# Kernel tuning notes

Measured on AMD Instinct MI355X. Metric: run time of the kernel, lower is better.

Reference implementation:

```python
import jax, jax.numpy as jnp
import numpy as np

B, T, C, H = 4, 4096, 2048, 128  # batch, seq, emb_dim, head_size


def setup_inputs() -> dict:
    key = jax.random.key(0)
    k1, k2, k3, k4 = jax.random.split(key, 4)
    idx = jax.random.normal(k1, (B, T, C), dtype=jnp.float32)
    # nn.Linear weight layout: [out_features, in_features]; scale like torch init
    s = 1.0 / np.sqrt(C)
    Wq = jax.random.uniform(k2, (H, C), jnp.float32, -s, s)
    Wk = jax.random.uniform(k3, (H, C), jnp.float32, -s, s)
    Wv = jax.random.uniform(k4, (H, C), jnp.float32, -s, s)
    return {"idx": idx, "Wq": Wq, "Wk": Wk, "Wv": Wv}


def reference(idx, Wq, Wk, Wv):
    b, t, c = idx.shape
    q = jnp.einsum('btc,hc->bth', idx, Wq)  # [B,T,H]
    k = jnp.einsum('btc,hc->bth', idx, Wk)
    v = jnp.einsum('btc,hc->bth', idx, Wv)
    # NOTE: original computes keys @ queries^T and scales by emb_dim**-0.5
    scale = jnp.asarray(c, idx.dtype) ** -0.5
    wei = jnp.einsum('bih,bjh->bij', k, q) * scale  # [B,T,T]
    causal = jnp.tril(jnp.ones((t, t), dtype=bool))
    wei = jnp.where(causal, wei, -jnp.inf)
    wei = jax.nn.softmax(wei, axis=-1)
    return jnp.einsum('bij,bjh->bih', wei, v)  # [B,T,H]
```

## Files before the change

kernel.cpp:

```cpp
#include <hip/hip_runtime.h>
#include <hip/hip_bf16.h>
#include <cstdint>

#define TSEQ 4096
#define CDIM 2048
#define HDIM 128

typedef short bf8v __attribute__((ext_vector_type(8)));
typedef float f4v  __attribute__((ext_vector_type(4)));

__device__ __forceinline__ unsigned short f2b(float f) {
  union { float f; unsigned u; } v; v.f = f;
  unsigned u = v.u;
  return (unsigned short)((u + 0x7fffu + ((u >> 16) & 1u)) >> 16);
}

__device__ __forceinline__ f4v mfma16(bf8v a, bf8v b, f4v c) {
  return __builtin_amdgcn_mfma_f32_16x16x32_bf16(a, b, c, 0, 0, 0);
}

__device__ __forceinline__ void gload_lds16(const void* g, void* l) {
  __builtin_amdgcn_global_load_lds(
      (const __attribute__((address_space(1))) unsigned int*)g,
      (__attribute__((address_space(3))) unsigned int*)l, 16, 0, 0);
}

__global__ void wcat_kernel(const float* __restrict__ Wq, const float* __restrict__ Wk,
                            const float* __restrict__ Wv, unsigned short* __restrict__ Wcat) {
  int e = (blockIdx.x * 256 + threadIdx.x) * 4;
  int n = e >> 11;
  int k = e & 2047;
  const float* src;
  if (n < 128)      src = Wq + (size_t)n * CDIM + k;
  else if (n < 256) src = Wk + (size_t)(n - 128) * CDIM + k;
  else              src = Wv + (size_t)(n - 256) * CDIM + k;
  float4 f = *(const float4*)src;
  ushort4 o;
  o.x = f2b(f.x); o.y = f2b(f.y); o.z = f2b(f.z); o.w = f2b(f.w);
  *(ushort4*)(Wcat + e) = o;
}

__global__ __launch_bounds__(512, 6) void proj_gemm(const float* __restrict__ A,
                                                    const unsigned short* __restrict__ Bw,
                                                    unsigned short* __restrict__ QB,
                                                    unsigned short* __restrict__ KA,
                                                    unsigned short* __restrict__ VB) {
  __shared__ union {
    struct { unsigned short As[2][64][72]; unsigned short Bs[2][128][64]; } st;
    unsigned short Ct[64][132];
  } sm;
  const int m0 = blockIdx.x * 64;
  const int y  = blockIdx.y;
  const int n0g = y * 128;
  const int tid = threadIdx.x;
  const int lane = tid & 63;
  const int w = tid >> 6;
  const int wm = (w & 1) * 32, wn = (w >> 1) * 32;
  const int llo = lane & 15, lhi = lane >> 4;

  f4v acc[2][2];
#pragma unroll
  for (int i = 0; i < 2; ++i)
#pragma unroll
    for (int j = 0; j < 2; ++j) acc[i][j] = (f4v){0.f, 0.f, 0.f, 0.f};

  const int ar0 = tid >> 4;
  const int ac0 = (tid & 15) * 4;
  const float* aptr0 = A + (size_t)(m0 + ar0) * CDIM + ac0;
  const float* aptr1 = A + (size_t)(m0 + 32 + ar0) * CDIM + ac0;

  const int brow = lane >> 3;
  const int bgs  = (lane & 7) ^ brow;
  const unsigned short* bptr = Bw + (size_t)(n0g + w * 16 + brow) * CDIM + bgs * 8;

  float4 fa0 = *(const float4*)(aptr0);
  float4 fa1 = *(const float4*)(aptr1);
  gload_lds16(bptr,            &sm.st.Bs[0][w * 16][0]);
  gload_lds16(bptr + 8 * CDIM, &sm.st.Bs[0][w * 16 + 8][0]);
  {
    ushort4 o0, o1;
    o0.x = f2b(fa0.x); o0.y = f2b(fa0.y); o0.z = f2b(fa0.z); o0.w = f2b(fa0.w);
    o1.x = f2b(fa1.x); o1.y = f2b(fa1.y); o1.z = f2b(fa1.z); o1.w = f2b(fa1.w);
    *(ushort4*)&sm.st.As[0][ar0][ac0]      = o0;
    *(ushort4*)&sm.st.As[0][32 + ar0][ac0] = o1;
  }

  for (int it = 0; it < 32; ++it) {
    const int cur = it & 1;
    __syncthreads();
    if (it < 31) {
      fa0 = *(const float4*)(aptr0 + (it + 1) * 64);
      fa1 = *(const float4*)(aptr1 + (it + 1) * 64);
      const int nxt = cur ^ 1;
      gload_lds16(bptr + (it + 1) * 64,            &sm.st.Bs[nxt][w * 16][0]);
      gload_lds16(bptr + 8 * CDIM + (it + 1) * 64, &sm.st.Bs[nxt][w * 16 + 8][0]);
    }
#pragma unroll
    for (int kk = 0; kk < 2; ++kk) {
      bf8v af[2], bfr[2];
      af[0] = *(const bf8v*)&sm.st.As[cur][wm + llo][kk * 32 + lhi * 8];
      af[1] = *(const bf8v*)&sm.st.As[cur][wm + 16 + llo][kk * 32 + lhi * 8];
      const int bofs = (((kk << 2) + lhi) ^ (llo & 7)) * 8;
      bfr[0] = *(const bf8v*)&sm.st.Bs[cur][wn + llo][bofs];
      bfr[1] = *(const bf8v*)&sm.st.Bs[cur][wn + 16 + llo][bofs];
#pragma unroll
      for (int i = 0; i < 2; ++i)
#pragma unroll
        for (int j = 0; j < 2; ++j) acc[i][j] = mfma16(af[i], bfr[j], acc[i][j]);
    }
    if (it < 31) {
      const int nxt = cur ^ 1;
      ushort4 o0, o1;
      o0.x = f2b(fa0.x); o0.y = f2b(fa0.y); o0.z = f2b(fa0.z); o0.w = f2b(fa0.w);
      o1.x = f2b(fa1.x); o1.y = f2b(fa1.y); o1.z = f2b(fa1.z); o1.w = f2b(fa1.w);
      *(ushort4*)&sm.st.As[nxt][ar0][ac0]      = o0;
      *(ushort4*)&sm.st.As[nxt][32 + ar0][ac0] = o1;
    }
  }
  __syncthreads();
#pragma unroll
  for (int i = 0; i < 2; ++i)
#pragma unroll
    for (int j = 0; j < 2; ++j)
#pragma unroll
      for (int r = 0; r < 4; ++r)
        sm.Ct[wm + i * 16 + lhi * 4 + r][wn + j * 16 + llo] = f2b(acc[i][j][r]);
  __syncthreads();
  if (y < 2) {
    unsigned short* dst = (y == 0) ? QB : KA;
    const size_t base16 = (size_t)(m0 >> 4);
#pragma unroll
    for (int p = 0; p < 2; ++p) {
      int g = p * 512 + tid;
      int t16l = g >> 8, kk = (g >> 6) & 3, ln = g & 63;
      int lo = ln & 15, hi = ln >> 4;
      bf8v v = *(const bf8v*)&sm.Ct[t16l * 16 + lo][kk * 32 + hi * 8];
      *(bf8v*)(dst + (((base16 + t16l) * 4 + kk) * 64 + ln) * 8) = v;
    }
  } else {
    const size_t base32 = (size_t)(m0 >> 5);
#pragma unroll
    for (int p = 0; p < 3; ++p) {
      int g = p * 512 + tid;
      if (g < 1152) {
        int jbl = g / 576;
        int ht  = (g % 576) >> 6;
        int ln  = g & 63;
        int lo = ln & 15, hi = ln >> 4;
        bf8v v;
        if (ht == 8) {
#pragma unroll
          for (int e = 0; e < 8; ++e) v[e] = (lo == 0) ? (short)0x3F80 : (short)0;
        } else {
#pragma unroll
          for (int e = 0; e < 8; ++e) v[e] = (short)sm.Ct[jbl * 32 + hi * 8 + e][ht * 16 + lo];
        }
        *(bf8v*)(VB + (((base32 + jbl) * 9 + ht) * 512 + (size_t)ln * 8)) = v;
      }
    }
  }
}

__global__ __launch_bounds__(256, 4) void attn6(const unsigned short* __restrict__ QB,
                                                const unsigned short* __restrict__ KA,
                                                const unsigned short* __restrict__ VB,
                                                float* __restrict__ out) {
  __shared__ union SM {
    unsigned short Ps[4][2][16][68];
    struct { float Om[4][16][68]; float Lm[4][16]; } mg;
  } sm;
  const int x = blockIdx.x;
  const int b = x & 3;
  const int u = x >> 2;
  const int g = u >> 6, r0 = u & 63;
  const int s = (g & 1) ? (g * 64 + 63 - r0) : (g * 64 + r0);
  const int lastjt = s >> 2;
  const int tid = threadIdx.x;
  const int w = tid >> 6, lane = tid & 63;
  const int llo = lane & 15, lhi = lane >> 4;
  const float scale = 0.022097086912079608f;

  bf8v aK[4];
  {
    const unsigned short* kp = KA + (size_t)(b * 256 + s) * 2048;
#pragma unroll
    for (int kk = 0; kk < 4; ++kk) aK[kk] = *(const bf8v*)(kp + (kk * 64 + lane) * 8);
  }

  f4v Oacc[9];
#pragma unroll
  for (int nt = 0; nt < 9; ++nt) Oacc[nt] = (f4v){0.f, 0.f, 0.f, 0.f};

  auto computeS = [&](int jtS, int buf) {
    const unsigned short* qp = QB + (size_t)(b * 256 + jtS * 4) * 2048;
#pragma unroll
    for (int ct = 0; ct < 4; ++ct) {
      f4v acc = (f4v){0.f, 0.f, 0.f, 0.f};
#pragma unroll
      for (int kk = 0; kk < 4; ++kk) {
        bf8v bq = *(const bf8v*)(qp + ((ct * 4 + kk) * 64 + lane) * 8);
        acc = mfma16(aK[kk], bq, acc);
      }
#pragma unroll
      for (int r = 0; r < 4; ++r) {
        float sv = acc[r];
        if (jtS == lastjt) {
          int j = jtS * 64 + ct * 16 + llo;
          int i = s * 16 + lhi * 4 + r;
          if (j > i) sv = -3.0e38f;
        }
        sm.Ps[w][buf][lhi * 4 + r][ct * 16 + llo] = f2b(__expf(sv * scale));
      }
    }
  };

  if (w <= lastjt) computeS(w, 0);
  int buf = 0;
  for (int jt = w; jt <= lastjt; jt += 4) {
    bf8v aP0 = *(const bf8v*)&sm.Ps[w][buf][llo][lhi * 8];
    bf8v aP1 = *(const bf8v*)&sm.Ps[w][buf][llo][32 + lhi * 8];
    if (jt + 4 <= lastjt) computeS(jt + 4, buf ^ 1);
    const unsigned short* vp = VB + (size_t)(b * 128 + jt * 2) * 4608;
#pragma unroll
    for (int nt = 0; nt < 9; ++nt) {
      f4v o = Oacc[nt];
      o = mfma16(aP0, *(const bf8v*)(vp + nt * 512 + (size_t)lane * 8), o);
      o = mfma16(aP1, *(const bf8v*)(vp + 4608 + nt * 512 + (size_t)lane * 8), o);
      Oacc[nt] = o;
    }
    buf ^= 1;
  }

#pragma unroll
  for (int half = 0; half < 2; ++half) {
    __syncthreads();
#pragma unroll
    for (int nt = 0; nt < 4; ++nt)
#pragma unroll
      for (int r = 0; r < 4; ++r)
        sm.mg.Om[w][lhi * 4 + r][nt * 16 + llo] = Oacc[half * 4 + nt][r];
    if (half == 0 && llo == 0) {
#pragma unroll
      for (int r = 0; r < 4; ++r) sm.mg.Lm[w][lhi * 4 + r] = Oacc[8][r];
    }
    __syncthreads();
    {
      int row = tid >> 4, c0 = (tid & 15) * 4;
      float L = sm.mg.Lm[0][row] + sm.mg.Lm[1][row] + sm.mg.Lm[2][row] + sm.mg.Lm[3][row];
      float inv = 1.0f / L;
      float* op = out + (size_t)(b * TSEQ + s * 16 + row) * HDIM + half * 64 + c0;
#pragma unroll
      for (int e = 0; e < 4; ++e) {
        float o = sm.mg.Om[0][row][c0 + e] + sm.mg.Om[1][row][c0 + e] +
                  sm.mg.Om[2][row][c0 + e] + sm.mg.Om[3][row][c0 + e];
        op[e] = o * inv;
      }
    }
  }
}

extern "C" void kernel_launch(void* const* d_in, const int* in_sizes, int n_in,
                              void* d_out, int out_size, void* d_ws, size_t ws_size,
                              hipStream_t stream) {
  const float* idx = (const float*)d_in[0];
  const float* Wq  = (const float*)d_in[1];
  const float* Wk  = (const float*)d_in[2];
  const float* Wv  = (const float*)d_in[3];
  float* out = (float*)d_out;
  char* ws = (char*)d_ws;
  unsigned short* Wcat = (unsigned short*)ws;
  unsigned short* QB   = (unsigned short*)(ws + ((size_t)2  << 20));
  unsigned short* KA   = (unsigned short*)(ws + ((size_t)7  << 20));
  unsigned short* VB   = (unsigned short*)(ws + ((size_t)12 << 20));

  wcat_kernel<<<768, 256, 0, stream>>>(Wq, Wk, Wv, Wcat);
  proj_gemm<<<dim3(256, 3), 512, 0, stream>>>(idx, Wcat, QB, KA, VB);
  attn6<<<1024, 256, 0, stream>>>(QB, KA, VB, out);
}
```

Before: 286.2 us.

## Process two query row tiles per attention block to reuse Q and V loads

The attention kernel now gives each block two adjacent 16-row tiles, and loads each Q and V fragment once to feed both tiles' MFMAs. This halves global and L2 traffic for Q and V per unit of work. The grid is halved, with a new pairing scheme to balance causal work, and launch bounds drop to two blocks per SM to fit the doubled registers. Separately, the projection GEMM's float-to-bf16 conversion uses the packed v_cvt_pk_bf16_f32 instruction instead of manual rounding. The cost is higher register pressure and lower occupancy, and the last tile of each pair does some masked extra work.

Result: slower. 300.9 us (+5.1%).

```diff
diff --git a/kernel.cpp b/kernel.cpp
--- a/kernel.cpp
+++ b/kernel.cpp
@@ -13,6 +13,12 @@
   union { float f; unsigned u; } v; v.f = f;
   unsigned u = v.u;
   return (unsigned short)((u + 0x7fffu + ((u >> 16) & 1u)) >> 16);
+}
+
+__device__ __forceinline__ unsigned cvtpk(float a, float b) {
+  unsigned r;
+  asm("v_cvt_pk_bf16_f32 %0, %1, %2" : "=v"(r) : "v"(a), "v"(b));
+  return r;
 }
 
 __device__ __forceinline__ f4v mfma16(bf8v a, bf8v b, f4v c) {
@@ -78,11 +84,11 @@
   gload_lds16(bptr,            &sm.st.Bs[0][w * 16][0]);
   gload_lds16(bptr + 8 * CDIM, &sm.st.Bs[0][w * 16 + 8][0]);
   {
-    ushort4 o0, o1;
-    o0.x = f2b(fa0.x); o0.y = f2b(fa0.y); o0.z = f2b(fa0.z); o0.w = f2b(fa0.w);
-    o1.x = f2b(fa1.x); o1.y = f2b(fa1.y); o1.z = f2b(fa1.z); o1.w = f2b(fa1.w);
-    *(ushort4*)&sm.st.As[0][ar0][ac0]      = o0;
-    *(ushort4*)&sm.st.As[0][32 + ar0][ac0] = o1;
+    uint2 p0, p1;
+    p0.x = cvtpk(fa0.x, fa0.y); p0.y = cvtpk(fa0.z, fa0.w);
+    p1.x = cvtpk(fa1.x, fa1.y); p1.y = cvtpk(fa1.z, fa1.w);
+    *(uint2*)&sm.st.As[0][ar0][ac0]      = p0;
+    *(uint2*)&sm.st.As[0][32 + ar0][ac0] = p1;
   }
 
   for (int it = 0; it < 32; ++it) {
@@ -110,11 +116,11 @@
     }
     if (it < 31) {
       const int nxt = cur ^ 1;
-      ushort4 o0, o1;
-      o0.x = f2b(fa0.x); o0.y = f2b(fa0.y); o0.z = f2b(fa0.z); o0.w = f2b(fa0.w);
-      o1.x = f2b(fa1.x); o1.y = f2b(fa1.y); o1.z = f2b(fa1.z); o1.w = f2b(fa1.w);
-      *(ushort4*)&sm.st.As[nxt][ar0][ac0]      = o0;
-      *(ushort4*)&sm.st.As[nxt][32 + ar0][ac0] = o1;
+      uint2 p0, p1;
+      p0.x = cvtpk(fa0.x, fa0.y); p0.y = cvtpk(fa0.z, fa0.w);
+      p1.x = cvtpk(fa1.x, fa1.y); p1.y = cvtpk(fa1.z, fa1.w);
+      *(uint2*)&sm.st.As[nxt][ar0][ac0]      = p0;
+      *(uint2*)&sm.st.As[nxt][32 + ar0][ac0] = p1;
     }
   }
   __syncthreads();
@@ -161,102 +167,124 @@
   }
 }
 
-__global__ __launch_bounds__(256, 4) void attn6(const unsigned short* __restrict__ QB,
+__global__ __launch_bounds__(256, 2) void attn7(const unsigned short* __restrict__ QB,
                                                 const unsigned short* __restrict__ KA,
                                                 const unsigned short* __restrict__ VB,
                                                 float* __restrict__ out) {
   __shared__ union SM {
-    unsigned short Ps[4][2][16][68];
+    unsigned short Ps[2][4][2][16][68];
     struct { float Om[4][16][68]; float Lm[4][16]; } mg;
   } sm;
   const int x = blockIdx.x;
   const int b = x & 3;
-  const int u = x >> 2;
-  const int g = u >> 6, r0 = u & 63;
-  const int s = (g & 1) ? (g * 64 + 63 - r0) : (g * 64 + r0);
-  const int lastjt = s >> 2;
+  const int t = x >> 2;
+  const int u = (t < 64) ? (2 * t) : (255 - 2 * t);
+  const int sA = u * 2;
+  const int lastjt = u >> 1;
   const int tid = threadIdx.x;
   const int w = tid >> 6, lane = tid & 63;
   const int llo = lane & 15, lhi = lane >> 4;
   const float scale = 0.022097086912079608f;
 
-  bf8v aK[4];
+  bf8v aKA[4], aKB[4];
   {
-    const unsigned short* kp = KA + (size_t)(b * 256 + s) * 2048;
-#pragma unroll
-    for (int kk = 0; kk < 4; ++kk) aK[kk] = *(const bf8v*)(kp + (kk * 64 + lane) * 8);
-  }
-
-  f4v Oacc[9];
-#pragma unroll
-  for (int nt = 0; nt < 9; ++nt) Oacc[nt] = (f4v){0.f, 0.f, 0.f, 0.f};
-
-  auto computeS = [&](int jtS, int buf) {
+    const unsigned short* kp = KA + (size_t)(b * 256 + sA) * 2048;
+#pragma unroll
+    for (int kk = 0; kk < 4; ++kk) {
+      aKA[kk] = *(const bf8v*)(kp + (kk * 64 + lane) * 8);
+      aKB[kk] = *(const bf8v*)(kp + 2048 + (kk * 64 + lane) * 8);
+    }
+  }
+
+  f4v OA[9], OB[9];
+#pragma unroll
+  for (int nt = 0; nt < 9; ++nt) {
+    OA[nt] = (f4v){0.f, 0.f, 0.f, 0.f};
+    OB[nt] = (f4v){0.f, 0.f, 0.f, 0.f};
+  }
+
+  auto computeS2 = [&](int jtS, int buf) {
     const unsigned short* qp = QB + (size_t)(b * 256 + jtS * 4) * 2048;
 #pragma unroll
     for (int ct = 0; ct < 4; ++ct) {
-      f4v acc = (f4v){0.f, 0.f, 0.f, 0.f};
+      f4v accA = (f4v){0.f, 0.f, 0.f, 0.f};
+      f4v accB = (f4v){0.f, 0.f, 0.f, 0.f};
 #pragma unroll
       for (int kk = 0; kk < 4; ++kk) {
         bf8v bq = *(const bf8v*)(qp + ((ct * 4 + kk) * 64 + lane) * 8);
-        acc = mfma16(aK[kk], bq, acc);
+        accA = mfma16(aKA[kk], bq, accA);
+        accB = mfma16(aKB[kk], bq, accB);
       }
 #pragma unroll
       for (int r = 0; r < 4; ++r) {
-        float sv = acc[r];
+        float svA = accA[r], svB = accB[r];
         if (jtS == lastjt) {
-          int j = jtS * 64 + ct * 16 + llo;
-          int i = s * 16 + lhi * 4 + r;
-          if (j > i) sv = -3.0e38f;
+          int j  = jtS * 64 + ct * 16 + llo;
+          int iA = sA * 16 + lhi * 4 + r;
+          if (j > iA)      svA = -3.0e38f;
+          if (j > iA + 16) svB = -3.0e38f;
         }
-        sm.Ps[w][buf][lhi * 4 + r][ct * 16 + llo] = f2b(__expf(sv * scale));
+        sm.Ps[0][w][buf][lhi * 4 + r][ct * 16 + llo] = f2b(__expf(svA * scale));
+        sm.Ps[1][w][buf][lhi * 4 + r][ct * 16 + llo] = f2b(__expf(svB * scale));
       }
     }
   };
 
-  if (w <= lastjt) computeS(w, 0);
+  if (w <= lastjt) computeS2(w, 0);
   int buf = 0;
   for (int jt = w; jt <= lastjt; jt += 4) {
-    bf8v aP0 = *(const bf8v*)&sm.Ps[w][buf][llo][lhi * 8];
-    bf8v aP1 = *(const bf8v*)&sm.Ps[w][buf][llo][32 + lhi * 8];
-    if (jt + 4 <= lastjt) computeS(jt + 4, buf ^ 1);
+    bf8v aP0A = *(const bf8v*)&sm.Ps[0][w][buf][llo][lhi * 8];
+    bf8v aP1A = *(const bf8v*)&sm.Ps[0][w][buf][llo][32 + lhi * 8];
+    bf8v aP0B = *(const bf8v*)&sm.Ps[1][w][buf][llo][lhi * 8];
+    bf8v aP1B = *(const bf8v*)&sm.Ps[1][w][buf][llo][32 + lhi * 8];
+    if (jt + 4 <= lastjt) computeS2(jt + 4, buf ^ 1);
     const unsigned short* vp = VB + (size_t)(b * 128 + jt * 2) * 4608;
 #pragma unroll
     for (int nt = 0; nt < 9; ++nt) {
-      f4v o = Oacc[nt];
-      o = mfma16(aP0, *(const bf8v*)(vp + nt * 512 + (size_t)lane * 8), o);
-      o = mfma16(aP1, *(const bf8v*)(vp + 4608 + nt * 512 + (size_t)lane * 8), o);
-      Oacc[nt] = o;
+      bf8v v0 = *(const bf8v*)(vp + nt * 512 + (size_t)lane * 8);
+      bf8v v1 = *(const bf8v*)(vp + 4608 + nt * 512 + (size_t)lane * 8);
+      f4v oa = OA[nt];
+      oa = mfma16(aP0A, v0, oa);
+      oa = mfma16(aP1A, v1, oa);
+      OA[nt] = oa;
+      f4v ob = OB[nt];
+      ob = mfma16(aP0B, v0, ob);
+      ob = mfma16(aP1B, v1, ob);
+      OB[nt] = ob;
     }
     buf ^= 1;
   }
 
-#pragma unroll
-  for (int half = 0; half < 2; ++half) {
-    __syncthreads();
-#pragma unroll
-    for (int nt = 0; nt < 4; ++nt)
-#pragma unroll
-      for (int r = 0; r < 4; ++r)
-        sm.mg.Om[w][lhi * 4 + r][nt * 16 + llo] = Oacc[half * 4 + nt][r];
-    if (half == 0 && llo == 0) {
-#pragma unroll
-      for (int r = 0; r < 4; ++r) sm.mg.Lm[w][lhi * 4 + r] = Oacc[8][r];
-    }
-    __syncthreads();
-    {
-      int row = tid >> 4, c0 = (tid & 15) * 4;
-      float L = sm.mg.Lm[0][row] + sm.mg.Lm[1][row] + sm.mg.Lm[2][row] + sm.mg.Lm[3][row];
-      float inv = 1.0f / L;
-      float* op = out + (size_t)(b * TSEQ + s * 16 + row) * HDIM + half * 64 + c0;
-#pragma unroll
-      for (int e = 0; e < 4; ++e) {
-        float o = sm.mg.Om[0][row][c0 + e] + sm.mg.Om[1][row][c0 + e] +
-                  sm.mg.Om[2][row][c0 + e] + sm.mg.Om[3][row][c0 + e];
-        op[e] = o * inv;
-      }
-    }
-  }
+  auto mergeOne = [&](const f4v (&O)[9], int sX) {
+#pragma unroll
+    for (int half = 0; half < 2; ++half) {
+      __syncthreads();
+#pragma unroll
+      for (int nt = 0; nt < 4; ++nt)
+#pragma unroll
+        for (int r = 0; r < 4; ++r)
+          sm.mg.Om[w][lhi * 4 + r][nt * 16 + llo] = O[half * 4 + nt][r];
+      if (half == 0 && llo == 0) {
+#pragma unroll
+        for (int r = 0; r < 4; ++r) sm.mg.Lm[w][lhi * 4 + r] = O[8][r];
+      }
+      __syncthreads();
+      {
+        int row = tid >> 4, c0 = (tid & 15) * 4;
+        float L = sm.mg.Lm[0][row] + sm.mg.Lm[1][row] + sm.mg.Lm[2][row] + sm.mg.Lm[3][row];
+        float inv = 1.0f / L;
+        float* op = out + (size_t)(b * TSEQ + sX * 16 + row) * HDIM + half * 64 + c0;
+#pragma unroll
+        for (int e = 0; e < 4; ++e) {
+          float o = sm.mg.Om[0][row][c0 + e] + sm.mg.Om[1][row][c0 + e] +
+                    sm.mg.Om[2][row][c0 + e] + sm.mg.Om[3][row][c0 + e];
+          op[e] = o * inv;
+        }
+      }
+    }
+  };
+  mergeOne(OA, sA);
+  mergeOne(OB, sA + 1);
 }
 
 extern "C" void kernel_launch(void* const* d_in, const int* in_sizes, int n_in,
@@ -275,5 +303,5 @@
 
   wcat_kernel<<<768, 256, 0, stream>>>(Wq, Wk, Wv, Wcat);
   proj_gemm<<<dim3(256, 3), 512, 0, stream>>>(idx, Wcat, QB, KA, VB);
-  attn6<<<1024, 256, 0, stream>>>(QB, KA, VB, out);
-}
+  attn7<<<512, 256, 0, stream>>>(QB, KA, VB, out);
+}
```
